# Kernel optimization log

Hardware: AMD Instinct MI355X
Metric: run time of the kernel (lower is better)

Reference implementation:

```python
import jax, jax.numpy as jnp
import numpy as np

LAYERS = 20
STACKS = 2
LPS = LAYERS // STACKS  # layers per stack -> dilations 2**(l % LPS)
OUT_CH = 256
RES_CH = 64
GATE_CH = 128
SKIP_CH = 256


def setup_inputs() -> dict:
    key = jax.random.key(0)
    ks = jax.random.split(key, 16)
    B, T = 8, 16000
    s = 0.05
    inp = {
        "x": jax.random.normal(ks[0], (B, OUT_CH, T), dtype=jnp.float32),
        # first causal conv (note: original code applies w_pre to the shifted
        # input twice -> output is 2*w_pre(pre); w_cur is unused, so omitted)
        "w_pre0": jax.random.normal(ks[1], (RES_CH, OUT_CH)) * s,
        "b_pre0": jax.random.normal(ks[2], (RES_CH,)) * s,
        # per-layer dilated conv (no bias), residual block, skip projection
        "w_dil_pre": jax.random.normal(ks[3], (LAYERS, GATE_CH, RES_CH)) * s,
        "w_dil_cur": jax.random.normal(ks[4], (LAYERS, GATE_CH, RES_CH)) * s,
        "bias_h": jax.random.normal(ks[5], (LAYERS, GATE_CH)) * s,
        "w_res": jax.random.normal(ks[6], (LAYERS, RES_CH, RES_CH)) * s,
        "b_res": jax.random.normal(ks[7], (LAYERS, RES_CH)) * s,
        "w_skip": jax.random.normal(ks[8], (LAYERS, SKIP_CH, RES_CH)) * s,
        "b_skip": jax.random.normal(ks[9], (LAYERS, SKIP_CH)) * s,
        # output head
        "w_relu": jax.random.normal(ks[10], (SKIP_CH, SKIP_CH)) * s,
        "b_relu": jax.random.normal(ks[11], (SKIP_CH,)) * s,
        "w_out": jax.random.normal(ks[12], (OUT_CH, SKIP_CH)) * s,
        "b_out": jax.random.normal(ks[13], (OUT_CH,)) * s,
    }
    return inp


def _shift_right(h, d):
    # causal shift: pad d zeros on the left along time, drop last d samples
    return jnp.pad(h, ((0, 0), (0, 0), (d, 0)))[:, :, :-d]


def reference(x, w_pre0, b_pre0, w_dil_pre, w_dil_cur, bias_h,
              w_res, b_res, w_skip, b_skip, w_relu, b_relu, w_out, b_out):
    # first causal conv: original Conv2X1 'casual' path computes
    # w_pre(pre) + w_pre(pre) = 2 * w_pre(pre)  (faithful to source)
    pre = _shift_right(x, 1)
    h = 2.0 * (jnp.einsum('rc,bct->brt', w_pre0, pre) + b_pre0[None, :, None])

    skip = jnp.zeros((x.shape[0], SKIP_CH, x.shape[2]), dtype=h.dtype)
    for l in range(LAYERS):
        d = 2 ** (l % LPS)
        h_pre = _shift_right(h, d)
        # dilated 2x1 conv = two channel-wise linears (no bias), summed with bias_h
        a = (jnp.einsum('gr,brt->bgt', w_dil_pre[l], h_pre)
             + jnp.einsum('gr,brt->bgt', w_dil_cur[l], h)
             + bias_h[l][None, :, None])
        g = jnp.tanh(a[:, :RES_CH]) * jax.nn.sigmoid(a[:, RES_CH:])
        res = jnp.einsum('rq,bqt->brt', w_res[l], g) + b_res[l][None, :, None]
        h = h + res
        skip = skip + jnp.einsum('sr,brt->bst', w_skip[l], g) + b_skip[l][None, :, None]

    o = jax.nn.relu(skip)
    o = jnp.einsum('ps,bst->bpt', w_relu, o) + b_relu[None, :, None]
    o = jax.nn.relu(o)
    logits = jnp.einsum('os,bst->bot', w_out, o) + b_out[None, :, None]
    return jax.nn.softmax(logits, axis=1)  # (B, out_channels, T)
```

## Files before the change

### kernel.cpp

```cpp
#include <hip/hip_runtime.h>
#include <math.h>

#define B_ 8
#define T_ 16000
#define NBT 250
#define HROWS 16512
#define NLAY 20

typedef __attribute__((ext_vector_type(8))) short bf16x8;
typedef __attribute__((ext_vector_type(4))) float f32x4;
typedef __attribute__((ext_vector_type(4))) short sh4;

__device__ __forceinline__ unsigned short f2bf(float f){
  unsigned u = __float_as_uint(f);
  u += 0x7fffu + ((u >> 16) & 1u);
  return (unsigned short)(u >> 16);
}
__device__ __forceinline__ float bf2f(unsigned short s){
  return __uint_as_float(((unsigned)s) << 16);
}
__device__ __forceinline__ void split2(float v, unsigned short& hi, unsigned short& lo){
  hi = f2bf(v);
  lo = f2bf(v - bf2f(hi));
}

#define MFMA(a,b,c) __builtin_amdgcn_mfma_f32_16x16x32_bf16((a),(b),(c),0,0,0)

__device__ __forceinline__ void gload16(const short* gsrc, short* ldst){
  __builtin_amdgcn_global_load_lds(
      (const __attribute__((address_space(1))) unsigned int*)gsrc,
      (__attribute__((address_space(3))) unsigned int*)ldst, 16, 0, 0);
}

__global__ void k_split(const float* __restrict__ src, short* __restrict__ hi,
                        short* __restrict__ lo, int n){
  int idx = blockIdx.x * 256 + threadIdx.x;
  if (idx < n){
    unsigned short h, l; split2(src[idx], h, l);
    hi[idx] = (short)h; lo[idx] = (short)l;
  }
}
__global__ void k_split_gate(const float* __restrict__ wdp, const float* __restrict__ wdc,
                             short* __restrict__ hi, short* __restrict__ lo){
  int idx = blockIdx.x * 256 + threadIdx.x;
  if (idx < NLAY*128*128){
    int l   = idx >> 14;
    int rem = idx & 16383;
    int row = rem >> 7;
    int k   = rem & 127;
    float v = (k < 64) ? wdp[(l*128 + row)*64 + k] : wdc[(l*128 + row)*64 + (k-64)];
    unsigned short h, lo16; split2(v, h, lo16);
    hi[idx] = (short)h; lo[idx] = (short)lo16;
  }
}
__global__ void k_pack_wsf(const float* __restrict__ wsk, short* __restrict__ wsf){
  int idx = blockIdx.x * 256 + threadIdx.x;
  if (idx < NLAY*8*2*2*64*8){
    int e    = idx & 7;
    int j    = (idx >> 3) & 63;
    int kb2  = (idx >> 9) & 1;
    int half = (idx >> 10) & 1;
    int w    = (idx >> 11) & 7;
    int l    = idx >> 14;
    int row  = w*32 + half*16 + (j & 15);
    int ch   = (kb2*4 + (j >> 4))*8 + e;
    wsf[idx] = (short)f2bf(wsk[((size_t)l*256 + row)*64 + ch]);
  }
}
__global__ void k_bsum(const float* __restrict__ bsk, float* __restrict__ bsum){
  int s = threadIdx.x;
  if (s < 256){
    float a = 0.f;
#pragma unroll
    for (int l = 0; l < NLAY; ++l) a += bsk[l*256 + s];
    bsum[s] = a;
  }
}
__global__ void k_zero_guard(short* __restrict__ hA, short* __restrict__ hB){
  int idx = blockIdx.x * 256 + threadIdx.x;
  if (idx < B_*512*128){
    int b = idx / (512*128);
    int rem = idx - b*(512*128);
    size_t off = (size_t)b*HROWS*128 + rem;
    hA[off] = 0; hB[off] = 0;
  }
}

__global__ __launch_bounds__(512) void k_head_in(
    const float* __restrict__ x, const short* __restrict__ wph,
    const short* __restrict__ wpl, const float* __restrict__ bias,
    short* __restrict__ h)
{
  __shared__ short SXh[64*256], SXl[64*256];
  const int tid = threadIdx.x;
  const int bb = blockIdx.x / NBT;
  const int t0 = (blockIdx.x % NBT) * 64;
  const int lane = tid & 63, w = tid >> 6;
  const int l16 = lane & 15, l4 = lane >> 4;

  const float* xb = x + (size_t)bb * 256 * T_;
  {
    int col = lane;
    int t = t0 + col - 1;
#pragma unroll
    for (int p = 0; p < 16; ++p){
      int k0 = w*32 + p*2;
      float v0 = (t >= 0) ? xb[(size_t)k0*T_ + t] : 0.f;
      float v1 = (t >= 0) ? xb[(size_t)(k0+1)*T_ + t] : 0.f;
      unsigned short h0,l0,h1,l1; split2(v0,h0,l0); split2(v1,h1,l1);
      int idx = col*256 + (k0 ^ ((col & 15) << 3));
      ((unsigned int*)SXh)[idx>>1] = (unsigned)h0 | ((unsigned)h1 << 16);
      ((unsigned int*)SXl)[idx>>1] = (unsigned)l0 | ((unsigned)l1 << 16);
    }
  }
  __syncthreads();

  const int mi = w & 3, nh = w >> 2;
  const int rowA = mi*16 + l16;
  const int rt0 = mi*16 + l4*4;
  bf16x8 Ah[8], Al[8];
#pragma unroll
  for (int kb = 0; kb < 8; ++kb){
    int ko = kb*32 + l4*8;
    Ah[kb] = *(const bf16x8*)(wph + (size_t)rowA*256 + ko);
    Al[kb] = *(const bf16x8*)(wpl + (size_t)rowA*256 + ko);
  }
  short* hb = h + ((size_t)bb*HROWS + 512)*128;
#pragma unroll
  for (int nt = 0; nt < 2; ++nt){
    int col = (nh*2 + nt)*16 + l16;
    f32x4 acc = {0.f,0.f,0.f,0.f};
#pragma unroll
    for (int kb = 0; kb < 8; ++kb){
      int ko = (kb*32 + l4*8) ^ (l16 << 3);
      bf16x8 bhv = *(const bf16x8*)&SXh[col*256 + ko];
      bf16x8 blv = *(const bf16x8*)&SXl[col*256 + ko];
      acc = MFMA(Ah[kb], bhv, acc);
      acc = MFMA(Ah[kb], blv, acc);
      acc = MFMA(Al[kb], bhv, acc);
    }
    int t = t0 + col;
    int key = t & 15;
    int c  = rt0 >> 3, sub = rt0 & 7;
    sh4 hv, lv;
#pragma unroll
    for (int r = 0; r < 4; ++r){
      float v = 2.f*(acc[r] + bias[rt0 + r]);
      unsigned short hh, ll; split2(v, hh, ll);
      hv[r] = (short)hh; lv[r] = (short)ll;
    }
    *(sh4*)&hb[(size_t)t*128 + ((c ^ key) << 3) + sub] = hv;
    *(sh4*)&hb[(size_t)t*128 + (((c + 8) ^ key) << 3) + sub] = lv;
  }
}

__global__ __launch_bounds__(512, 6) void k_layer6(
    const short* __restrict__ hin, short* __restrict__ hout,
    short* __restrict__ gout,
    const short* __restrict__ wgh, const short* __restrict__ wgl,
    const short* __restrict__ wrh, const short* __restrict__ wrlo,
    const float* __restrict__ bh, const float* __restrict__ br, int d)
{
  __shared__ short SH[64*128];
  __shared__ short SHP[64*128];
  const int tid = threadIdx.x;
  const int bb = blockIdx.x / NBT;
  const int tile = blockIdx.x % NBT;
  const int t0 = tile * 64;
  const int lane = tid & 63, w = tid >> 6;
  const int l16 = lane & 15, l4 = lane >> 4;

  const short* hb = hin + ((size_t)bb*HROWS + 512)*128;
  {
#pragma unroll
    for (int i = 0; i < 2; ++i){
      int colb = (w*2 + i)*4;
      const short* s1 = hb + (size_t)(t0 + colb + (lane>>4))*128 + (lane&15)*8;
      gload16(s1, &SH[colb*128]);
      const short* s2 = hb + (size_t)(t0 - d + colb + (lane>>4))*128 + (lane&15)*8;
      gload16(s2, &SHP[colb*128]);
    }
  }

  const int mi = w & 3, nh = w >> 2;
  const int rt0 = mi*16 + l4*4;
  const int rowt = mi*16 + l16, rows = 64 + mi*16 + l16;
  float bt[4], bs[4];
#pragma unroll
  for (int r = 0; r < 4; ++r){ bt[r] = bh[rt0+r]; bs[r] = bh[64+rt0+r]; }
  __syncthreads();

  f32x4 at0 = {0.f,0.f,0.f,0.f}, at1 = {0.f,0.f,0.f,0.f};
  f32x4 as0 = {0.f,0.f,0.f,0.f}, as1 = {0.f,0.f,0.f,0.f};
  {
#pragma unroll
    for (int kb = 0; kb < 2; ++kb){
      int ko = kb*32 + l4*8;
      bf16x8 Wth = *(const bf16x8*)(wgh + (size_t)rowt*128 + ko);
      bf16x8 Wtl = *(const bf16x8*)(wgl + (size_t)rowt*128 + ko);
      bf16x8 Wsh = *(const bf16x8*)(wgh + (size_t)rows*128 + ko);
      bf16x8 Wsl = *(const bf16x8*)(wgl + (size_t)rows*128 + ko);
      int cb = kb*4 + l4;
#pragma unroll
      for (int nt = 0; nt < 2; ++nt){
        int col = (nh*2 + nt)*16 + l16;
        int keyP = (col - d) & 15;
        bf16x8 bhv = *(const bf16x8*)&SHP[col*128 + ((cb ^ keyP) << 3)];
        bf16x8 blv = *(const bf16x8*)&SHP[col*128 + (((cb + 8) ^ keyP) << 3)];
        if (nt == 0){
          at0 = MFMA(Wth, bhv, at0); at0 = MFMA(Wth, blv, at0); at0 = MFMA(Wtl, bhv, at0);
          as0 = MFMA(Wsh, bhv, as0); as0 = MFMA(Wsh, blv, as0); as0 = MFMA(Wsl, bhv, as0);
        } else {
          at1 = MFMA(Wth, bhv, at1); at1 = MFMA(Wth, blv, at1); at1 = MFMA(Wtl, bhv, at1);
          as1 = MFMA(Wsh, bhv, as1); as1 = MFMA(Wsh, blv, as1); as1 = MFMA(Wsl, bhv, as1);
        }
      }
    }
  }
  {
#pragma unroll
    for (int kb = 2; kb < 4; ++kb){
      int ko = kb*32 + l4*8;
      bf16x8 Wth = *(const bf16x8*)(wgh + (size_t)rowt*128 + ko);
      bf16x8 Wtl = *(const bf16x8*)(wgl + (size_t)rowt*128 + ko);
      bf16x8 Wsh = *(const bf16x8*)(wgh + (size_t)rows*128 + ko);
      bf16x8 Wsl = *(const bf16x8*)(wgl + (size_t)rows*128 + ko);
      int cb = (kb & 1)*4 + l4;
#pragma unroll
      for (int nt = 0; nt < 2; ++nt){
        int col = (nh*2 + nt)*16 + l16;
        int keyC = col & 15;
        bf16x8 bhv = *(const bf16x8*)&SH[col*128 + ((cb ^ keyC) << 3)];
        bf16x8 blv = *(const bf16x8*)&SH[col*128 + (((cb + 8) ^ keyC) << 3)];
        if (nt == 0){
          at0 = MFMA(Wth, bhv, at0); at0 = MFMA(Wth, blv, at0); at0 = MFMA(Wtl, bhv, at0);
          as0 = MFMA(Wsh, bhv, as0); as0 = MFMA(Wsh, blv, as0); as0 = MFMA(Wsl, bhv, as0);
        } else {
          at1 = MFMA(Wth, bhv, at1); at1 = MFMA(Wth, blv, at1); at1 = MFMA(Wtl, bhv, at1);
          as1 = MFMA(Wsh, bhv, as1); as1 = MFMA(Wsh, blv, as1); as1 = MFMA(Wsl, bhv, as1);
        }
      }
    }
  }

  unsigned gp[2][4];
#pragma unroll
  for (int nt = 0; nt < 2; ++nt){
    unsigned short gh4[4], gl4[4];
#pragma unroll
    for (int r = 0; r < 4; ++r){
      float av = ((nt == 0) ? at0[r] : at1[r]) + bt[r];
      float sv = ((nt == 0) ? as0[r] : as1[r]) + bs[r];
      float e2 = __expf(2.f*av);
      float tv = 1.f - 2.f/(e2 + 1.f);
      float sg = 1.f/(1.f + __expf(-sv));
      float g  = tv*sg;
      split2(g, gh4[r], gl4[r]);
    }
    gp[nt][0] = (unsigned)gh4[0] | ((unsigned)gh4[1] << 16);
    gp[nt][1] = (unsigned)gh4[2] | ((unsigned)gh4[3] << 16);
    gp[nt][2] = (unsigned)gl4[0] | ((unsigned)gl4[1] << 16);
    gp[nt][3] = (unsigned)gl4[2] | ((unsigned)gl4[3] << 16);
  }
  __syncthreads();

  short* SGh = SHP;
  short* SGl = SHP + 4096;
#pragma unroll
  for (int nt = 0; nt < 2; ++nt){
    int col = (nh*2 + nt)*16 + l16;
    int gib = col*64 + (rt0 ^ ((col & 7) << 3));
    ((unsigned int*)&SGh[gib])[0] = gp[nt][0];
    ((unsigned int*)&SGh[gib])[1] = gp[nt][1];
    ((unsigned int*)&SGl[gib])[0] = gp[nt][2];
    ((unsigned int*)&SGl[gib])[1] = gp[nt][3];
  }
  __syncthreads();

  {
    int f = tid >> 6, j = tid & 63;
    int row = (f >> 1)*16 + (j & 15);
    int c   = (f & 1)*4 + (j >> 4);
    bf16x8 v = *(const bf16x8*)&SGh[row*64 + ((c ^ (row & 7)) << 3)];
    *(bf16x8*)(gout + ((size_t)bb*NBT + tile)*4096 + tid*8) = v;
  }

  {
    const int rowA = mi*16 + l16;
    bf16x8 Rh[2], Rl[2];
#pragma unroll
    for (int kb = 0; kb < 2; ++kb){
      int ko = kb*32 + l4*8;
      Rh[kb] = *(const bf16x8*)(wrh  + (size_t)rowA*64 + ko);
      Rl[kb] = *(const bf16x8*)(wrlo + (size_t)rowA*64 + ko);
    }
    short* ho = hout + ((size_t)bb*HROWS + 512)*128;
    const int cH = rt0 >> 3, sub = rt0 & 7;
#pragma unroll
    for (int nt = 0; nt < 2; ++nt){
      int col = (nh*2 + nt)*16 + l16;
      int keyC = col & 15;
      f32x4 acc = {0.f,0.f,0.f,0.f};
#pragma unroll
      for (int kb = 0; kb < 2; ++kb){
        int ko = (kb*32 + l4*8) ^ ((col & 7) << 3);
        bf16x8 bhv = *(const bf16x8*)&SGh[col*64 + ko];
        bf16x8 blv = *(const bf16x8*)&SGl[col*64 + ko];
        acc = MFMA(Rh[kb], bhv, acc);
        acc = MFMA(Rh[kb], blv, acc);
        acc = MFMA(Rl[kb], bhv, acc);
      }
      sh4 hi4 = *(const sh4*)&SH[col*128 + ((cH ^ keyC) << 3) + sub];
      sh4 lo4 = *(const sh4*)&SH[col*128 + (((cH + 8) ^ keyC) << 3) + sub];
      int t = t0 + col;
      sh4 hv, lv;
#pragma unroll
      for (int r = 0; r < 4; ++r){
        float hin_f = bf2f((unsigned short)hi4[r]) + bf2f((unsigned short)lo4[r]);
        float v = hin_f + acc[r] + br[rt0 + r];
        unsigned short hh, ll; split2(v, hh, ll);
        hv[r] = (short)hh; lv[r] = (short)ll;
      }
      *(sh4*)&ho[(size_t)t*128 + ((cH ^ keyC) << 3) + sub] = hv;
      *(sh4*)&ho[(size_t)t*128 + (((cH + 8) ^ keyC) << 3) + sub] = lv;
    }
  }
}

__global__ __launch_bounds__(512) void k_head_fused(
    float* __restrict__ io,
    const short* __restrict__ g,
    const short* __restrict__ wsf,
    const float* __restrict__ bsum,
    const short* __restrict__ wrlh, const short* __restrict__ wrll,
    const float* __restrict__ brl,
    const short* __restrict__ woh, const short* __restrict__ wol,
    const float* __restrict__ bo)
{
  __shared__ short POOL[16384];
  const int tid = threadIdx.x;
  const int bb = blockIdx.x / NBT;
  const int tile = blockIdx.x % NBT;
  const int t0 = tile * 64;
  const int lane = tid & 63, w = tid >> 6;
  const int l16 = lane & 15, l4 = lane >> 4;

  const int r0 = w*32 + l16, r1 = w*32 + 16 + l16;
  const int rtb0 = w*32 + l4*4, rtb1 = rtb0 + 16;

  f32x4 acc0[4], acc1[4];
#pragma unroll
  for (int nt = 0; nt < 4; ++nt){ acc0[nt] = (f32x4){0.f,0.f,0.f,0.f}; acc1[nt] = (f32x4){0.f,0.f,0.f,0.f}; }

  {
    const size_t LSTR = (size_t)B_ * NBT * 4096;
    const short* gtile = g + ((size_t)bb*NBT + tile)*4096;
    const short* wb = wsf + (size_t)w*2048 + lane*8;

#define STAGE(l20, buf) gload16(gtile + (size_t)(l20)*LSTR + w*512 + lane*8, &POOL[(buf)*4096 + w*512])

    STAGE(0, 0);
    for (int l20 = 0; l20 < 20; ++l20){
      const short* wl = wb + (size_t)l20*16384;
      bf16x8 A00 = *(const bf16x8*)(wl);
      bf16x8 A01 = *(const bf16x8*)(wl + 512);
      bf16x8 A10 = *(const bf16x8*)(wl + 1024);
      bf16x8 A11 = *(const bf16x8*)(wl + 1536);
      if (l20 + 1 < 20){
        STAGE(l20 + 1, (l20 + 1) & 1);
        asm volatile("s_waitcnt vmcnt(1)" ::: "memory");
      } else {
        asm volatile("s_waitcnt vmcnt(0)" ::: "memory");
      }
      __builtin_amdgcn_s_barrier();
      __builtin_amdgcn_sched_barrier(0);
      const short* gt = &POOL[(l20 & 1)*4096];
#pragma unroll
      for (int nt = 0; nt < 4; ++nt){
        bf16x8 B0 = *(const bf16x8*)(gt + (nt*2    )*512 + lane*8);
        bf16x8 B1 = *(const bf16x8*)(gt + (nt*2 + 1)*512 + lane*8);
        acc0[nt] = MFMA(A00, B0, acc0[nt]);
        acc0[nt] = MFMA(A01, B1, acc0[nt]);
        acc1[nt] = MFMA(A10, B0, acc1[nt]);
        acc1[nt] = MFMA(A11, B1, acc1[nt]);
      }
      __builtin_amdgcn_sched_barrier(0);
      __builtin_amdgcn_s_barrier();
    }
#undef STAGE
  }

  short* S1h = POOL;
  {
    float bs0[4], bs1[4];
#pragma unroll
    for (int r = 0; r < 4; ++r){ bs0[r] = bsum[rtb0+r]; bs1[r] = bsum[rtb1+r]; }
#pragma unroll
    for (int nt = 0; nt < 4; ++nt){
      int c2 = nt*16 + l16;
      unsigned short h[4];
#pragma unroll
      for (int r = 0; r < 4; ++r)
        h[r] = f2bf(fmaxf(acc0[nt][r] + bs0[r], 0.f));
      int i0 = c2*256 + (rtb0 ^ (l16 << 3));
      ((unsigned int*)&S1h[i0])[0] = (unsigned)h[0] | ((unsigned)h[1] << 16);
      ((unsigned int*)&S1h[i0])[1] = (unsigned)h[2] | ((unsigned)h[3] << 16);
#pragma unroll
      for (int r = 0; r < 4; ++r)
        h[r] = f2bf(fmaxf(acc1[nt][r] + bs1[r], 0.f));
      int i1 = c2*256 + (rtb1 ^ (l16 << 3));
      ((unsigned int*)&S1h[i1])[0] = (unsigned)h[0] | ((unsigned)h[1] << 16);
      ((unsigned int*)&S1h[i1])[1] = (unsigned)h[2] | ((unsigned)h[3] << 16);
    }
  }
  __syncthreads();

#pragma unroll
  for (int nt = 0; nt < 4; ++nt){ acc0[nt] = (f32x4){0.f,0.f,0.f,0.f}; acc1[nt] = (f32x4){0.f,0.f,0.f,0.f}; }
#pragma unroll
  for (int kb = 0; kb < 8; ++kb){
    int ko = kb*32 + l4*8;
    bf16x8 A0h = *(const bf16x8*)(wrlh + (size_t)r0*256 + ko);
    bf16x8 A0l = *(const bf16x8*)(wrll + (size_t)r0*256 + ko);
    bf16x8 A1h = *(const bf16x8*)(wrlh + (size_t)r1*256 + ko);
    bf16x8 A1l = *(const bf16x8*)(wrll + (size_t)r1*256 + ko);
#pragma unroll
    for (int nt = 0; nt < 4; ++nt){
      int c2 = nt*16 + l16;
      int kos = ko ^ (l16 << 3);
      bf16x8 bhv = *(const bf16x8*)&S1h[c2*256 + kos];
      acc0[nt] = MFMA(A0h, bhv, acc0[nt]);
      acc0[nt] = MFMA(A0l, bhv, acc0[nt]);
      acc1[nt] = MFMA(A1h, bhv, acc1[nt]);
      acc1[nt] = MFMA(A1l, bhv, acc1[nt]);
    }
  }
  __syncthreads();
  {
    float br0[4], br1[4];
#pragma unroll
    for (int r = 0; r < 4; ++r){ br0[r] = brl[rtb0+r]; br1[r] = brl[rtb1+r]; }
#pragma unroll
    for (int nt = 0; nt < 4; ++nt){
      int c2 = nt*16 + l16;
      unsigned short h[4];
#pragma unroll
      for (int r = 0; r < 4; ++r)
        h[r] = f2bf(fmaxf(acc0[nt][r] + br0[r], 0.f));
      int i0 = c2*256 + (rtb0 ^ (l16 << 3));
      ((unsigned int*)&S1h[i0])[0] = (unsigned)h[0] | ((unsigned)h[1] << 16);
      ((unsigned int*)&S1h[i0])[1] = (unsigned)h[2] | ((unsigned)h[3] << 16);
#pragma unroll
      for (int r = 0; r < 4; ++r)
        h[r] = f2bf(fmaxf(acc1[nt][r] + br1[r], 0.f));
      int i1 = c2*256 + (rtb1 ^ (l16 << 3));
      ((unsigned int*)&S1h[i1])[0] = (unsigned)h[0] | ((unsigned)h[1] << 16);
      ((unsigned int*)&S1h[i1])[1] = (unsigned)h[2] | ((unsigned)h[3] << 16);
    }
  }
  __syncthreads();

#pragma unroll
  for (int nt = 0; nt < 4; ++nt){ acc0[nt] = (f32x4){0.f,0.f,0.f,0.f}; acc1[nt] = (f32x4){0.f,0.f,0.f,0.f}; }
#pragma unroll
  for (int kb = 0; kb < 8; ++kb){
    int ko = kb*32 + l4*8;
    bf16x8 A0h = *(const bf16x8*)(woh + (size_t)r0*256 + ko);
    bf16x8 A0l = *(const bf16x8*)(wol + (size_t)r0*256 + ko);
    bf16x8 A1h = *(const bf16x8*)(woh + (size_t)r1*256 + ko);
    bf16x8 A1l = *(const bf16x8*)(wol + (size_t)r1*256 + ko);
#pragma unroll
    for (int nt = 0; nt < 4; ++nt){
      int c2 = nt*16 + l16;
      int kos = ko ^ (l16 << 3);
      bf16x8 bhv = *(const bf16x8*)&S1h[c2*256 + kos];
      acc0[nt] = MFMA(A0h, bhv, acc0[nt]);
      acc0[nt] = MFMA(A0l, bhv, acc0[nt]);
      acc1[nt] = MFMA(A1h, bhv, acc1[nt]);
      acc1[nt] = MFMA(A1l, bhv, acc1[nt]);
    }
  }
  __syncthreads();
  float* smax = (float*)POOL;
  float* ssum = smax + 512;
  float* iob = io + (size_t)bb * 256 * T_;
  float bo0[4], bo1[4];
#pragma unroll
  for (int r = 0; r < 4; ++r){ bo0[r] = bo[rtb0+r]; bo1[r] = bo[rtb1+r]; }
#pragma unroll
  for (int nt = 0; nt < 4; ++nt){
    float m = -1e30f;
#pragma unroll
    for (int r = 0; r < 4; ++r){
      acc0[nt][r] += bo0[r];
      acc1[nt][r] += bo1[r];
      m = fmaxf(m, fmaxf(acc0[nt][r], acc1[nt][r]));
    }
    m = fmaxf(m, __shfl_xor(m, 16, 64));
    m = fmaxf(m, __shfl_xor(m, 32, 64));
    smax[w*64 + nt*16 + l16] = m;
  }
  __syncthreads();
#pragma unroll
  for (int nt = 0; nt < 4; ++nt){
    float m = smax[nt*16 + l16];
#pragma unroll
    for (int ww = 1; ww < 8; ++ww) m = fmaxf(m, smax[ww*64 + nt*16 + l16]);
    float s = 0.f;
#pragma unroll
    for (int r = 0; r < 4; ++r){
      acc0[nt][r] = __expf(acc0[nt][r] - m); s += acc0[nt][r];
      acc1[nt][r] = __expf(acc1[nt][r] - m); s += acc1[nt][r];
    }
    s += __shfl_xor(s, 16, 64);
    s += __shfl_xor(s, 32, 64);
    ssum[w*64 + nt*16 + l16] = s;
  }
  __syncthreads();
#pragma unroll
  for (int nt = 0; nt < 4; ++nt){
    float S = 0.f;
#pragma unroll
    for (int ww = 0; ww < 8; ++ww) S += ssum[ww*64 + nt*16 + l16];
    float inv = 1.f / S;
    int t = t0 + nt*16 + l16;
#pragma unroll
    for (int r = 0; r < 4; ++r){
      iob[(size_t)(rtb0 + r)*T_ + t] = acc0[nt][r]*inv;
      iob[(size_t)(rtb1 + r)*T_ + t] = acc1[nt][r]*inv;
    }
  }
}

extern "C" void kernel_launch(void* const* d_in, const int* in_sizes, int n_in,
                              void* d_out, int out_size, void* d_ws, size_t ws_size,
                              hipStream_t stream) {
  const float* x       = (const float*)d_in[0];
  const float* w_pre0  = (const float*)d_in[1];
  const float* b_pre0  = (const float*)d_in[2];
  const float* w_dil_p = (const float*)d_in[3];
  const float* w_dil_c = (const float*)d_in[4];
  const float* bias_h  = (const float*)d_in[5];
  const float* w_res   = (const float*)d_in[6];
  const float* b_res   = (const float*)d_in[7];
  const float* w_skip  = (const float*)d_in[8];
  const float* b_skip  = (const float*)d_in[9];
  const float* w_relu  = (const float*)d_in[10];
  const float* b_relu  = (const float*)d_in[11];
  const float* w_out   = (const float*)d_in[12];
  const float* b_out   = (const float*)d_in[13];

  float* out = (float*)d_out;
  short* hA = (short*)d_ws;
  short* hB = hA + (size_t)B_ * HROWS * 128;
  float* bsum = (float*)(hB + (size_t)B_ * HROWS * 128);
  short* p   = (short*)(bsum + 256);
  short* WPh = p; p += 16384;  short* WPl = p; p += 16384;
  short* WGh = p; p += 327680; short* WGl = p; p += 327680;
  short* WRh = p; p += 81920;  short* WRl = p; p += 81920;
  short* WSF = p; p += 327680;
  short* WLh = p; p += 65536;  short* WLl = p; p += 65536;
  short* WOh = p; p += 65536;  short* WOl = p; p += 65536;
  short* GBUF = p;

  k_split<<<64, 256, 0, stream>>>(w_pre0, WPh, WPl, 16384);
  k_split_gate<<<1280, 256, 0, stream>>>(w_dil_p, w_dil_c, WGh, WGl);
  k_split<<<320, 256, 0, stream>>>(w_res, WRh, WRl, 81920);
  k_pack_wsf<<<1280, 256, 0, stream>>>(w_skip, WSF);
  k_split<<<256, 256, 0, stream>>>(w_relu, WLh, WLl, 65536);
  k_split<<<256, 256, 0, stream>>>(w_out, WOh, WOl, 65536);
  k_zero_guard<<<2048, 256, 0, stream>>>(hA, hB);
  k_bsum<<<1, 256, 0, stream>>>(b_skip, bsum);

  k_head_in<<<B_ * NBT, 512, 0, stream>>>(x, WPh, WPl, b_pre0, hA);

  const short* hin = hA;
  short* houtp = hB;
  for (int l = 0; l < NLAY; ++l) {
    int d = 1 << (l % 10);
    k_layer6<<<B_ * NBT, 512, 0, stream>>>(
        hin, houtp,
        GBUF + (size_t)l * B_ * NBT * 4096,
        WGh + (size_t)l*16384, WGl + (size_t)l*16384,
        WRh + (size_t)l*4096,  WRl + (size_t)l*4096,
        bias_h + (size_t)l*128, b_res + (size_t)l*64, d);
    const short* tmp = hin;
    hin = houtp;
    houtp = (short*)tmp;
  }

  k_head_fused<<<B_ * NBT, 512, 0, stream>>>(
      out, GBUF, WSF, bsum, WLh, WLl, b_relu, WOh, WOl, b_out);
}
```

Measured before the change: 1.328 ms.

## Load skip-sum gate fragments directly into registers, dropping LDS staging and barriers

The skip accumulation phase of the fused head kernel no longer stages gate tiles through double-buffered shared memory with barriers. Each wave now loads its own B fragments straight from global memory and computes an 8-row-block by one-column-tile slab, reading more weight fragments per layer. This removes the LDS round trip and the per-layer block synchronisation. In exchange there is more global and L2 traffic for weights, and global load latency is no longer explicitly overlapped with compute.

Result: slower. 1.494 ms (+12.5%).

```diff
diff --git a/kernel.cpp b/kernel.cpp
--- a/kernel.cpp
+++ b/kernel.cpp
@@ -337,7 +337,7 @@
     const short* __restrict__ woh, const short* __restrict__ wol,
     const float* __restrict__ bo)
 {
-  __shared__ short POOL[16384];
+  __shared__ short S1h[64*256];
   const int tid = threadIdx.x;
   const int bb = blockIdx.x / NBT;
   const int tile = blockIdx.x % NBT;
@@ -348,73 +348,46 @@
   const int r0 = w*32 + l16, r1 = w*32 + 16 + l16;
   const int rtb0 = w*32 + l4*4, rtb1 = rtb0 + 16;
 
-  f32x4 acc0[4], acc1[4];
-#pragma unroll
-  for (int nt = 0; nt < 4; ++nt){ acc0[nt] = (f32x4){0.f,0.f,0.f,0.f}; acc1[nt] = (f32x4){0.f,0.f,0.f,0.f}; }
-
+  const int rh = w >> 2, ntw = w & 3;
+  f32x4 acc[8];
+#pragma unroll
+  for (int m = 0; m < 8; ++m) acc[m] = (f32x4){0.f,0.f,0.f,0.f};
   {
     const size_t LSTR = (size_t)B_ * NBT * 4096;
-    const short* gtile = g + ((size_t)bb*NBT + tile)*4096;
-    const short* wb = wsf + (size_t)w*2048 + lane*8;
-
-#define STAGE(l20, buf) gload16(gtile + (size_t)(l20)*LSTR + w*512 + lane*8, &POOL[(buf)*4096 + w*512])
-
-    STAGE(0, 0);
+    const short* gfrag = g + ((size_t)bb*NBT + tile)*4096 + (ntw*2)*512 + lane*8;
+    const short* wbase = wsf + (size_t)rh*4*2048 + lane*8;
     for (int l20 = 0; l20 < 20; ++l20){
-      const short* wl = wb + (size_t)l20*16384;
-      bf16x8 A00 = *(const bf16x8*)(wl);
-      bf16x8 A01 = *(const bf16x8*)(wl + 512);
-      bf16x8 A10 = *(const bf16x8*)(wl + 1024);
-      bf16x8 A11 = *(const bf16x8*)(wl + 1536);
-      if (l20 + 1 < 20){
-        STAGE(l20 + 1, (l20 + 1) & 1);
-        asm volatile("s_waitcnt vmcnt(1)" ::: "memory");
-      } else {
-        asm volatile("s_waitcnt vmcnt(0)" ::: "memory");
+      bf16x8 B0 = *(const bf16x8*)(gfrag + (size_t)l20*LSTR);
+      bf16x8 B1 = *(const bf16x8*)(gfrag + (size_t)l20*LSTR + 512);
+      const short* wl = wbase + (size_t)l20*16384;
+#pragma unroll
+      for (int m = 0; m < 8; ++m){
+        const short* wm = wl + (m >> 1)*2048 + (m & 1)*1024;
+        bf16x8 A0 = *(const bf16x8*)(wm);
+        bf16x8 A1 = *(const bf16x8*)(wm + 512);
+        acc[m] = MFMA(A0, B0, acc[m]);
+        acc[m] = MFMA(A1, B1, acc[m]);
       }
-      __builtin_amdgcn_s_barrier();
-      __builtin_amdgcn_sched_barrier(0);
-      const short* gt = &POOL[(l20 & 1)*4096];
-#pragma unroll
-      for (int nt = 0; nt < 4; ++nt){
-        bf16x8 B0 = *(const bf16x8*)(gt + (nt*2    )*512 + lane*8);
-        bf16x8 B1 = *(const bf16x8*)(gt + (nt*2 + 1)*512 + lane*8);
-        acc0[nt] = MFMA(A00, B0, acc0[nt]);
-        acc0[nt] = MFMA(A01, B1, acc0[nt]);
-        acc1[nt] = MFMA(A10, B0, acc1[nt]);
-        acc1[nt] = MFMA(A11, B1, acc1[nt]);
-      }
-      __builtin_amdgcn_sched_barrier(0);
-      __builtin_amdgcn_s_barrier();
-    }
-#undef STAGE
-  }
-
-  short* S1h = POOL;
-  {
-    float bs0[4], bs1[4];
-#pragma unroll
-    for (int r = 0; r < 4; ++r){ bs0[r] = bsum[rtb0+r]; bs1[r] = bsum[rtb1+r]; }
-#pragma unroll
-    for (int nt = 0; nt < 4; ++nt){
-      int c2 = nt*16 + l16;
+    }
+  }
+
+  {
+    const int c2 = ntw*16 + l16;
+#pragma unroll
+    for (int m = 0; m < 8; ++m){
+      int rtb = rh*128 + m*16 + l4*4;
       unsigned short h[4];
 #pragma unroll
       for (int r = 0; r < 4; ++r)
-        h[r] = f2bf(fmaxf(acc0[nt][r] + bs0[r], 0.f));
-      int i0 = c2*256 + (rtb0 ^ (l16 << 3));
+        h[r] = f2bf(fmaxf(acc[m][r] + bsum[rtb + r], 0.f));
+      int i0 = c2*256 + (rtb ^ (l16 << 3));
       ((unsigned int*)&S1h[i0])[0] = (unsigned)h[0] | ((unsigned)h[1] << 16);
       ((unsigned int*)&S1h[i0])[1] = (unsigned)h[2] | ((unsigned)h[3] << 16);
-#pragma unroll
-      for (int r = 0; r < 4; ++r)
-        h[r] = f2bf(fmaxf(acc1[nt][r] + bs1[r], 0.f));
-      int i1 = c2*256 + (rtb1 ^ (l16 << 3));
-      ((unsigned int*)&S1h[i1])[0] = (unsigned)h[0] | ((unsigned)h[1] << 16);
-      ((unsigned int*)&S1h[i1])[1] = (unsigned)h[2] | ((unsigned)h[3] << 16);
-    }
-  }
-  __syncthreads();
-
+    }
+  }
+  __syncthreads();
+
+  f32x4 acc0[4], acc1[4];
 #pragma unroll
   for (int nt = 0; nt < 4; ++nt){ acc0[nt] = (f32x4){0.f,0.f,0.f,0.f}; acc1[nt] = (f32x4){0.f,0.f,0.f,0.f}; }
 #pragma unroll
@@ -481,7 +454,7 @@
     }
   }
   __syncthreads();
-  float* smax = (float*)POOL;
+  float* smax = (float*)S1h;
   float* ssum = smax + 512;
   float* iob = io + (size_t)bb * 256 * T_;
   float bo0[4], bo1[4];
```
